# Kernel optimization log

Measured on AMD Instinct MI355X. Metric: run time of the kernel, lower is better.

The kernel has to match this reference:

```python
import jax, jax.numpy as jnp
import numpy as np

B, T, D = 2, 4096, 768
H = 12
DK = D // H


def setup_inputs() -> dict:
    key = jax.random.key(0)
    k1, k2, k3 = jax.random.split(key, 3)
    x = jax.random.normal(k1, (B, T, D), dtype=jnp.float32)
    W_qkv = jax.random.normal(k2, (D, 3 * D), dtype=jnp.float32) * (1.0 / np.sqrt(D))
    b_qkv = jnp.zeros((3 * D,), dtype=jnp.float32)
    W_proj = jax.random.normal(k3, (D, D), dtype=jnp.float32) * (1.0 / np.sqrt(D))
    b_proj = jnp.zeros((D,), dtype=jnp.float32)
    return {"x": x, "W_qkv": W_qkv, "b_qkv": b_qkv, "W_proj": W_proj, "b_proj": b_proj}


def reference(x, W_qkv, b_qkv, W_proj, b_proj):
    b, t, c = x.shape
    qkv = x @ W_qkv + b_qkv                      # [B,T,3D]
    q, k, v = jnp.split(qkv, 3, axis=-1)
    q = q.reshape(b, t, H, DK)                   # [B,T,H,DK]
    k = k.reshape(b, t, H, DK)
    v = v.reshape(b, t, H, DK)
    scale = 1.0 / np.sqrt(DK)
    scores = jnp.einsum('bthd,bshd->bhts', q, k) * scale   # [B,H,T,T]
    causal = jnp.tril(jnp.ones((t, t), dtype=bool))
    scores = jnp.where(causal[None, None], scores, jnp.float32(-jnp.inf))
    probs = jax.nn.softmax(scores, axis=-1)      # dropout p=0.0 -> identity
    out = jnp.einsum('bhts,bshd->bthd', probs, v).reshape(b, t, c)
    return out @ W_proj + b_proj
```

## Files before the change

### kernel.cpp

```cpp
#include <hip/hip_runtime.h>
#include <hip/hip_bf16.h>
#include <cstdint>
#include <cstddef>


typedef __attribute__((ext_vector_type(8))) short bf16x8;
typedef __attribute__((ext_vector_type(4))) float f32x4;

#define MFMA16(a, b, c) __builtin_amdgcn_mfma_f32_16x16x32_bf16((a), (b), (c), 0, 0, 0)

static constexpr int Bc = 2, Tc = 4096, Dc = 768, Hc = 12, DKc = 64;
static constexpr int BHc = Bc * Hc;
static constexpr int Mc = Bc * Tc;
static constexpr int Nqkv = 3 * Dc;
static constexpr int NQBLK = Tc / 128;
static constexpr unsigned int NITEMS = BHc * NQBLK;

__device__ __forceinline__ unsigned short f2bf(float f) {
    union { float f; unsigned int i; } c; c.f = f;
    unsigned int x = c.i;
    return (unsigned short)((x + 0x7fffu + ((x >> 16) & 1u)) >> 16);
}
__device__ __forceinline__ unsigned int pkbf(float a, float b) {
    __hip_bfloat162 h = __float22bfloat162_rn(make_float2(a, b));
    union { __hip_bfloat162 h; unsigned int u; } c; c.h = h;
    return c.u;
}

__global__ __launch_bounds__(256)
void xconv_kernel(const float* __restrict__ X, unsigned short* __restrict__ Xb) {
    size_t i = ((size_t)blockIdx.x * 256 + threadIdx.x) * 8;
    float4 a = *(const float4*)(X + i);
    float4 b = *(const float4*)(X + i + 4);
    uint4 o;
    o.x = pkbf(a.x, a.y); o.y = pkbf(a.z, a.w);
    o.z = pkbf(b.x, b.y); o.w = pkbf(b.z, b.w);
    *(uint4*)(Xb + i) = o;
}

__global__ __launch_bounds__(256)
void wtrans_kernel(const float* __restrict__ W, unsigned short* __restrict__ WT,
                   int K, int N) {
    __shared__ __align__(16) unsigned short tile[64 * 72];
    const int k0 = blockIdx.x * 64;
    const int n0 = blockIdx.y * 64;
    const int tid = threadIdx.x;
#pragma unroll
    for (int it = 0; it < 4; ++it) {
        int s = tid + it * 256;
        int r = s >> 4, g = s & 15;
        float4 v = *(const float4*)(W + (size_t)(k0 + r) * N + n0 + g * 4);
        ushort4 u;
        u.x = f2bf(v.x); u.y = f2bf(v.y); u.z = f2bf(v.z); u.w = f2bf(v.w);
        *(ushort4*)(tile + r * 72 + g * 4) = u;
    }
    __syncthreads();
#pragma unroll
    for (int it = 0; it < 2; ++it) {
        int s = tid + it * 256;
        int n = s >> 3, g = s & 7;
        unsigned int p0 = (unsigned int)tile[(g * 8 + 0) * 72 + n] |
                          ((unsigned int)tile[(g * 8 + 1) * 72 + n] << 16);
        unsigned int p1 = (unsigned int)tile[(g * 8 + 2) * 72 + n] |
                          ((unsigned int)tile[(g * 8 + 3) * 72 + n] << 16);
        unsigned int p2 = (unsigned int)tile[(g * 8 + 4) * 72 + n] |
                          ((unsigned int)tile[(g * 8 + 5) * 72 + n] << 16);
        unsigned int p3 = (unsigned int)tile[(g * 8 + 6) * 72 + n] |
                          ((unsigned int)tile[(g * 8 + 7) * 72 + n] << 16);
        uint4 o; o.x = p0; o.y = p1; o.z = p2; o.w = p3;
        *(uint4*)(WT + (size_t)(n0 + n) * K + k0 + g * 8) = o;
    }
}

__global__ __launch_bounds__(256)
void qkv_gemm_kernel(const unsigned short* __restrict__ Xb,
                     const unsigned short* __restrict__ WT,
                     const float* __restrict__ bias,
                     unsigned short* __restrict__ Qb, unsigned short* __restrict__ Kb,
                     unsigned short* __restrict__ Vt) {
    __shared__ __align__(16) unsigned short As[128 * 40];
    __shared__ __align__(16) unsigned short Bs[128 * 40];
    const int tid = threadIdx.x;
    const int wave = tid >> 6, lane = tid & 63;
    const int quad = lane >> 4, l15 = lane & 15;
    const int wr = wave >> 1, wc = wave & 1;
    const int r0 = blockIdx.x * 128, c0 = blockIdx.y * 128;

    f32x4 acc[4][4];
#pragma unroll
    for (int i = 0; i < 4; ++i)
#pragma unroll
        for (int j = 0; j < 4; ++j) acc[i][j] = (f32x4){0.f, 0.f, 0.f, 0.f};

    for (int k0 = 0; k0 < Dc; k0 += 32) {
#pragma unroll
        for (int it = 0; it < 2; ++it) {
            int s = tid + it * 256;
            int r = s >> 2, g = s & 3;
            *(uint4*)(As + r * 40 + g * 8) =
                *(const uint4*)(Xb + (size_t)(r0 + r) * Dc + k0 + g * 8);
            *(uint4*)(Bs + r * 40 + g * 8) =
                *(const uint4*)(WT + (size_t)(c0 + r) * Dc + k0 + g * 8);
        }
        __syncthreads();
        bf16x8 af[4], bfr[4];
#pragma unroll
        for (int mt = 0; mt < 4; ++mt)
            af[mt] = *(const bf16x8*)(As + (wr * 64 + mt * 16 + l15) * 40 + quad * 8);
#pragma unroll
        for (int nt = 0; nt < 4; ++nt)
            bfr[nt] = *(const bf16x8*)(Bs + (wc * 64 + nt * 16 + l15) * 40 + quad * 8);
#pragma unroll
        for (int mt = 0; mt < 4; ++mt)
#pragma unroll
            for (int nt = 0; nt < 4; ++nt)
                acc[mt][nt] = MFMA16(af[mt], bfr[nt], acc[mt][nt]);
        __syncthreads();
    }

    const int part = c0 / Dc;
    const int cbase = c0 - part * Dc;
    const float scale = (part == 0) ? 0.125f : 1.0f;
    float bv[4];
#pragma unroll
    for (int nt = 0; nt < 4; ++nt) bv[nt] = bias[c0 + wc * 64 + nt * 16 + l15];

    if (part < 2) {
        unsigned short* dstbuf = (part == 0) ? Qb : Kb;
#pragma unroll
        for (int mt = 0; mt < 4; ++mt)
#pragma unroll
            for (int reg = 0; reg < 4; ++reg) {
                int gr = r0 + wr * 64 + mt * 16 + quad * 4 + reg;
                int b = gr >> 12, t = gr & 4095;
#pragma unroll
                for (int nt = 0; nt < 4; ++nt) {
                    int cc = cbase + wc * 64 + nt * 16 + l15;
                    int h = cc >> 6, dk = cc & 63;
                    float v = (acc[mt][nt][reg] + bv[nt]) * scale;
                    dstbuf[((size_t)(b * Hc + h) * Tc + t) * DKc + dk] = f2bf(v);
                }
            }
    } else {
#pragma unroll
        for (int mt = 0; mt < 4; ++mt)
#pragma unroll
            for (int reg = 0; reg < 4; ++reg) {
                int gr = r0 + wr * 64 + mt * 16 + quad * 4 + reg;
                int b = gr >> 12, t = gr & 4095;
#pragma unroll
                for (int nt = 0; nt < 4; ++nt) {
                    int cc = cbase + wc * 64 + nt * 16 + l15;
                    int h = cc >> 6, dk = cc & 63;
                    float v = acc[mt][nt][reg] + bv[nt];
                    Vt[((size_t)(b * Hc + h) * DKc + dk) * Tc + t] = f2bf(v);
                }
            }
    }
}

__global__ __launch_bounds__(256)
void attn_kernel(const unsigned short* __restrict__ Qb,
                 const unsigned short* __restrict__ Kb,
                 const unsigned short* __restrict__ Vt,
                 unsigned short* __restrict__ attn,
                 unsigned int* __restrict__ counter) {
    __shared__ __align__(16) unsigned short Ks[64 * 72];
    __shared__ __align__(16) unsigned short Vs[64 * 72];
    __shared__ __align__(16) unsigned short Ps[4 * 16 * 72];
    __shared__ float Linv[128];
    __shared__ unsigned int s_w;
    const int tid = threadIdx.x;
    const int wave = tid >> 6, lane = tid & 63;
    const int quad = lane >> 4, l15 = lane & 15;
    const int rr = tid >> 3, gg = tid & 7;
    unsigned short* Pw = Ps + wave * 16 * 72;

    for (;;) {
        if (tid == 0) s_w = atomicAdd(counter, 1u);
        __syncthreads();
        const unsigned int w = s_w;
        if (w >= NITEMS) break;
        const int bh = (int)(w % (unsigned)BHc);
        const int i0 = (NQBLK - 1 - (int)(w / (unsigned)BHc)) * 128;
        const unsigned short* Qp = Qb + (size_t)bh * Tc * DKc;
        const unsigned short* Kp = Kb + (size_t)bh * Tc * DKc;
        const unsigned short* Vp = Vt + (size_t)bh * DKc * Tc;

        bf16x8 qf[2][2];
#pragma unroll
        for (int qg = 0; qg < 2; ++qg)
#pragma unroll
            for (int f = 0; f < 2; ++f)
                qf[qg][f] = *(const bf16x8*)(Qp +
                    (size_t)(i0 + wave * 32 + qg * 16 + l15) * DKc + f * 32 + quad * 8);

        f32x4 lp[2] = {(f32x4){0.f,0.f,0.f,0.f}, (f32x4){0.f,0.f,0.f,0.f}};
        f32x4 o[2][4];
#pragma unroll
        for (int qg = 0; qg < 2; ++qg)
#pragma unroll
            for (int nt = 0; nt < 4; ++nt) o[qg][nt] = (f32x4){0.f, 0.f, 0.f, 0.f};

        const int jmax = (i0 >> 6) + 1;
        for (int jt = 0; jt <= jmax; ++jt) {
            const int j0 = jt * 64;
#pragma unroll
            for (int it = 0; it < 2; ++it) {
                int r = rr + it * 32;
                *(uint4*)(Ks + r * 72 + gg * 8) =
                    *(const uint4*)(Kp + (size_t)(j0 + r) * DKc + gg * 8);
                *(uint4*)(Vs + r * 72 + gg * 8) =
                    *(const uint4*)(Vp + (size_t)r * Tc + j0 + gg * 8);
            }
            __syncthreads();

            bf16x8 kf[2][4], vf[2][4];
#pragma unroll
            for (int f = 0; f < 2; ++f)
#pragma unroll
                for (int mt = 0; mt < 4; ++mt)
                    kf[f][mt] = *(const bf16x8*)(Ks + (mt * 16 + l15) * 72 + f * 32 + quad * 8);
#pragma unroll
            for (int f = 0; f < 2; ++f)
#pragma unroll
                for (int nt = 0; nt < 4; ++nt)
                    vf[f][nt] = *(const bf16x8*)(Vs + (nt * 16 + l15) * 72 + f * 32 + quad * 8);

            const int rel = j0 - i0;
            const bool maskit = (jt >= jmax - 1);
#pragma unroll
            for (int qg = 0; qg < 2; ++qg) {
                f32x4 sc[4];
#pragma unroll
                for (int mt = 0; mt < 4; ++mt) sc[mt] = (f32x4){0.f, 0.f, 0.f, 0.f};
#pragma unroll
                for (int f = 0; f < 2; ++f)
#pragma unroll
                    for (int mt = 0; mt < 4; ++mt)
                        sc[mt] = MFMA16(kf[f][mt], qf[qg][f], sc[mt]);

                if (maskit) {
                    int qrow = wave * 32 + qg * 16 + l15;
#pragma unroll
                    for (int mt = 0; mt < 4; ++mt)
#pragma unroll
                        for (int reg = 0; reg < 4; ++reg)
                            if (rel + mt * 16 + quad * 4 + reg > qrow)
                                sc[mt][reg] = -1e30f;
                }

#pragma unroll
                for (int mt = 0; mt < 4; ++mt) {
#pragma unroll
                    for (int reg = 0; reg < 4; ++reg)
                        sc[mt][reg] = __expf(sc[mt][reg]);
                    lp[qg] += sc[mt];
                }

#pragma unroll
                for (int mt = 0; mt < 4; ++mt) {
                    uint2 u;
                    u.x = pkbf(sc[mt][0], sc[mt][1]);
                    u.y = pkbf(sc[mt][2], sc[mt][3]);
                    *(uint2*)(Pw + l15 * 72 + mt * 16 + quad * 4) = u;
                }

#pragma unroll
                for (int f = 0; f < 2; ++f) {
                    bf16x8 pf = *(const bf16x8*)(Pw + l15 * 72 + f * 32 + quad * 8);
#pragma unroll
                    for (int nt = 0; nt < 4; ++nt)
                        o[qg][nt] = MFMA16(pf, vf[f][nt], o[qg][nt]);
                }
            }
            __syncthreads();
        }

#pragma unroll
        for (int qg = 0; qg < 2; ++qg) {
            float ls = lp[qg][0] + lp[qg][1] + lp[qg][2] + lp[qg][3];
            ls += __shfl_xor(ls, 16);
            ls += __shfl_xor(ls, 32);
            Linv[wave * 32 + qg * 16 + l15] = 1.0f / ls;
        }

        const int b = bh / Hc, h = bh % Hc;
#pragma unroll
        for (int qg = 0; qg < 2; ++qg) {
            f32x4 li = *(const f32x4*)(Linv + wave * 32 + qg * 16 + quad * 4);
#pragma unroll
            for (int nt = 0; nt < 4; ++nt)
#pragma unroll
                for (int reg = 0; reg < 4; ++reg) {
                    int t = i0 + wave * 32 + qg * 16 + quad * 4 + reg;
                    attn[(size_t)(b * Tc + t) * Dc + h * 64 + nt * 16 + l15] =
                        f2bf(o[qg][nt][reg] * li[reg]);
                }
        }
        __syncthreads();
    }
}

__global__ __launch_bounds__(256)
void proj_gemm_kernel(const unsigned short* __restrict__ A,
                      const unsigned short* __restrict__ WT,
                      const float* __restrict__ bias, float* __restrict__ out) {
    __shared__ __align__(16) unsigned short As[128 * 40];
    __shared__ __align__(16) unsigned short Bs[128 * 40];
    const int tid = threadIdx.x;
    const int wave = tid >> 6, lane = tid & 63;
    const int quad = lane >> 4, l15 = lane & 15;
    const int wr = wave >> 1, wc = wave & 1;
    const int r0 = blockIdx.x * 128, c0 = blockIdx.y * 128;

    f32x4 acc[4][4];
#pragma unroll
    for (int i = 0; i < 4; ++i)
#pragma unroll
        for (int j = 0; j < 4; ++j) acc[i][j] = (f32x4){0.f, 0.f, 0.f, 0.f};

    for (int k0 = 0; k0 < Dc; k0 += 32) {
#pragma unroll
        for (int it = 0; it < 2; ++it) {
            int s = tid + it * 256;
            int r = s >> 2, g = s & 3;
            *(uint4*)(As + r * 40 + g * 8) =
                *(const uint4*)(A + (size_t)(r0 + r) * Dc + k0 + g * 8);
            *(uint4*)(Bs + r * 40 + g * 8) =
                *(const uint4*)(WT + (size_t)(c0 + r) * Dc + k0 + g * 8);
        }
        __syncthreads();
        bf16x8 af[4], bfr[4];
#pragma unroll
        for (int mt = 0; mt < 4; ++mt)
            af[mt] = *(const bf16x8*)(As + (wr * 64 + mt * 16 + l15) * 40 + quad * 8);
#pragma unroll
        for (int nt = 0; nt < 4; ++nt)
            bfr[nt] = *(const bf16x8*)(Bs + (wc * 64 + nt * 16 + l15) * 40 + quad * 8);
#pragma unroll
        for (int mt = 0; mt < 4; ++mt)
#pragma unroll
            for (int nt = 0; nt < 4; ++nt)
                acc[mt][nt] = MFMA16(af[mt], bfr[nt], acc[mt][nt]);
        __syncthreads();
    }

    float bv[4];
#pragma unroll
    for (int nt = 0; nt < 4; ++nt) bv[nt] = bias[c0 + wc * 64 + nt * 16 + l15];
#pragma unroll
    for (int mt = 0; mt < 4; ++mt)
#pragma unroll
        for (int reg = 0; reg < 4; ++reg) {
            int gr = r0 + wr * 64 + mt * 16 + quad * 4 + reg;
#pragma unroll
            for (int nt = 0; nt < 4; ++nt) {
                int gc = c0 + wc * 64 + nt * 16 + l15;
                out[(size_t)gr * Dc + gc] = acc[mt][nt][reg] + bv[nt];
            }
        }
}

extern "C" void kernel_launch(void* const* d_in, const int* in_sizes, int n_in,
                              void* d_out, int out_size, void* d_ws, size_t ws_size,
                              hipStream_t stream) {
    const float* x      = (const float*)d_in[0];
    const float* W_qkv  = (const float*)d_in[1];
    const float* b_qkv  = (const float*)d_in[2];
    const float* W_proj = (const float*)d_in[3];
    const float* b_proj = (const float*)d_in[4];
    float* out = (float*)d_out;

    char* ws = (char*)d_ws;
    size_t off = 0;
    auto take = [&](size_t bytes) -> char* {
        char* p = ws + off;
        off += (bytes + 255) & ~(size_t)255;
        return p;
    };
    unsigned int*   cnt = (unsigned int*)take(256);
    unsigned short* WqT = (unsigned short*)take((size_t)Nqkv * Dc * 2);
    unsigned short* WpT = (unsigned short*)take((size_t)Dc * Dc * 2);
    unsigned short* Qb  = (unsigned short*)take((size_t)BHc * Tc * DKc * 2);
    unsigned short* Kb  = (unsigned short*)take((size_t)BHc * Tc * DKc * 2);
    unsigned short* Vt  = (unsigned short*)take((size_t)BHc * Tc * DKc * 2);
    unsigned short* Xb  = (unsigned short*)take((size_t)Mc * Dc * 2);
    unsigned short* An  = Xb;

    hipMemsetAsync(cnt, 0, sizeof(unsigned int), stream);
    xconv_kernel<<<dim3((Mc * Dc) / (256 * 8)), dim3(256), 0, stream>>>(x, Xb);
    wtrans_kernel<<<dim3(Dc / 64, Nqkv / 64), dim3(256), 0, stream>>>(W_qkv, WqT, Dc, Nqkv);
    wtrans_kernel<<<dim3(Dc / 64, Dc / 64), dim3(256), 0, stream>>>(W_proj, WpT, Dc, Dc);
    qkv_gemm_kernel<<<dim3(Mc / 128, Nqkv / 128), dim3(256), 0, stream>>>(Xb, WqT, b_qkv, Qb, Kb, Vt);
    attn_kernel<<<dim3(NITEMS), dim3(256), 0, stream>>>(Qb, Kb, Vt, An, cnt);
    proj_gemm_kernel<<<dim3(Mc / 128, Dc / 128), dim3(256), 0, stream>>>(An, WpT, b_proj, out);
}
```

Before: 291.3 us.

## Make attention wave-independent with register-resident P and direct global K/V loads

Restructures the attention kernel so each wave pulls its own 32-query work item from the atomic counter and loads K and V fragments straight from global memory. This removes shared-memory staging and all block barriers. The P matrix now stays in registers and feeds a 16x16x16 MFMA with V as the A operand, avoiding the LDS round trip. Log2(e) is folded into the Q scale so exp2 replaces expf, and launch bounds request 3 blocks per CU. The trade-off is that K/V reuse across waves now relies on cache instead of LDS, which raises global/L2 traffic.

Measured after the change: 603.6 us. 107% more time.

```diff
diff --git a/kernel.cpp b/kernel.cpp
--- a/kernel.cpp
+++ b/kernel.cpp
@@ -5,16 +5,17 @@
 
 
 typedef __attribute__((ext_vector_type(8))) short bf16x8;
+typedef __attribute__((ext_vector_type(4))) short bf16x4;
 typedef __attribute__((ext_vector_type(4))) float f32x4;
 
-#define MFMA16(a, b, c) __builtin_amdgcn_mfma_f32_16x16x32_bf16((a), (b), (c), 0, 0, 0)
+#define MFMA16(a, b, c)   __builtin_amdgcn_mfma_f32_16x16x32_bf16((a), (b), (c), 0, 0, 0)
+#define MFMA16K(a, b, c)  __builtin_amdgcn_mfma_f32_16x16x16bf16_1k((a), (b), (c), 0, 0, 0)
 
 static constexpr int Bc = 2, Tc = 4096, Dc = 768, Hc = 12, DKc = 64;
 static constexpr int BHc = Bc * Hc;
 static constexpr int Mc = Bc * Tc;
 static constexpr int Nqkv = 3 * Dc;
-static constexpr int NQBLK = Tc / 128;
-static constexpr unsigned int NITEMS = BHc * NQBLK;
+static constexpr unsigned int NITEMS = BHc * (Tc / 32);
 
 __device__ __forceinline__ unsigned short f2bf(float f) {
     union { float f; unsigned int i; } c; c.f = f;
@@ -120,7 +121,7 @@
 
     const int part = c0 / Dc;
     const int cbase = c0 - part * Dc;
-    const float scale = (part == 0) ? 0.125f : 1.0f;
+    const float scale = (part == 0) ? 0.125f * 1.4426950408889634f : 1.0f;
     float bv[4];
 #pragma unroll
     for (int nt = 0; nt < 4; ++nt) bv[nt] = bias[c0 + wc * 64 + nt * 16 + l15];
@@ -159,30 +160,22 @@
     }
 }
 
-__global__ __launch_bounds__(256)
+__global__ __launch_bounds__(256, 3)
 void attn_kernel(const unsigned short* __restrict__ Qb,
                  const unsigned short* __restrict__ Kb,
                  const unsigned short* __restrict__ Vt,
                  unsigned short* __restrict__ attn,
                  unsigned int* __restrict__ counter) {
-    __shared__ __align__(16) unsigned short Ks[64 * 72];
-    __shared__ __align__(16) unsigned short Vs[64 * 72];
-    __shared__ __align__(16) unsigned short Ps[4 * 16 * 72];
-    __shared__ float Linv[128];
-    __shared__ unsigned int s_w;
-    const int tid = threadIdx.x;
-    const int wave = tid >> 6, lane = tid & 63;
+    const int lane = threadIdx.x & 63;
     const int quad = lane >> 4, l15 = lane & 15;
-    const int rr = tid >> 3, gg = tid & 7;
-    unsigned short* Pw = Ps + wave * 16 * 72;
 
     for (;;) {
-        if (tid == 0) s_w = atomicAdd(counter, 1u);
-        __syncthreads();
-        const unsigned int w = s_w;
+        unsigned int w = 0;
+        if (lane == 0) w = atomicAdd(counter, 1u);
+        w = (unsigned int)__shfl((int)w, 0);
         if (w >= NITEMS) break;
         const int bh = (int)(w % (unsigned)BHc);
-        const int i0 = (NQBLK - 1 - (int)(w / (unsigned)BHc)) * 128;
+        const int i0 = (Tc / 32 - 1 - (int)(w / (unsigned)BHc)) * 32;
         const unsigned short* Qp = Qb + (size_t)bh * Tc * DKc;
         const unsigned short* Kp = Kb + (size_t)bh * Tc * DKc;
         const unsigned short* Vp = Vt + (size_t)bh * DKc * Tc;
@@ -193,112 +186,89 @@
 #pragma unroll
             for (int f = 0; f < 2; ++f)
                 qf[qg][f] = *(const bf16x8*)(Qp +
-                    (size_t)(i0 + wave * 32 + qg * 16 + l15) * DKc + f * 32 + quad * 8);
+                    (size_t)(i0 + qg * 16 + l15) * DKc + f * 32 + quad * 8);
 
         f32x4 lp[2] = {(f32x4){0.f,0.f,0.f,0.f}, (f32x4){0.f,0.f,0.f,0.f}};
         f32x4 o[2][4];
 #pragma unroll
         for (int qg = 0; qg < 2; ++qg)
 #pragma unroll
-            for (int nt = 0; nt < 4; ++nt) o[qg][nt] = (f32x4){0.f, 0.f, 0.f, 0.f};
-
-        const int jmax = (i0 >> 6) + 1;
+            for (int d = 0; d < 4; ++d) o[qg][d] = (f32x4){0.f, 0.f, 0.f, 0.f};
+
+        const int jmax = i0 >> 6;
         for (int jt = 0; jt <= jmax; ++jt) {
             const int j0 = jt * 64;
-#pragma unroll
-            for (int it = 0; it < 2; ++it) {
-                int r = rr + it * 32;
-                *(uint4*)(Ks + r * 72 + gg * 8) =
-                    *(const uint4*)(Kp + (size_t)(j0 + r) * DKc + gg * 8);
-                *(uint4*)(Vs + r * 72 + gg * 8) =
-                    *(const uint4*)(Vp + (size_t)r * Tc + j0 + gg * 8);
-            }
-            __syncthreads();
-
-            bf16x8 kf[2][4], vf[2][4];
+
+            f32x4 sc[2][4];
+#pragma unroll
+            for (int qg = 0; qg < 2; ++qg)
+#pragma unroll
+                for (int mt = 0; mt < 4; ++mt) sc[qg][mt] = (f32x4){0.f, 0.f, 0.f, 0.f};
 #pragma unroll
             for (int f = 0; f < 2; ++f)
 #pragma unroll
-                for (int mt = 0; mt < 4; ++mt)
-                    kf[f][mt] = *(const bf16x8*)(Ks + (mt * 16 + l15) * 72 + f * 32 + quad * 8);
-#pragma unroll
-            for (int f = 0; f < 2; ++f)
-#pragma unroll
-                for (int nt = 0; nt < 4; ++nt)
-                    vf[f][nt] = *(const bf16x8*)(Vs + (nt * 16 + l15) * 72 + f * 32 + quad * 8);
-
-            const int rel = j0 - i0;
-            const bool maskit = (jt >= jmax - 1);
-#pragma unroll
-            for (int qg = 0; qg < 2; ++qg) {
-                f32x4 sc[4];
-#pragma unroll
-                for (int mt = 0; mt < 4; ++mt) sc[mt] = (f32x4){0.f, 0.f, 0.f, 0.f};
-#pragma unroll
-                for (int f = 0; f < 2; ++f)
+                for (int mt = 0; mt < 4; ++mt) {
+                    bf16x8 kf = *(const bf16x8*)(Kp +
+                        (size_t)(j0 + mt * 16 + l15) * DKc + f * 32 + quad * 8);
+                    sc[0][mt] = MFMA16(kf, qf[0][f], sc[0][mt]);
+                    sc[1][mt] = MFMA16(kf, qf[1][f], sc[1][mt]);
+                }
+
+            if (jt == jmax) {
+#pragma unroll
+                for (int qg = 0; qg < 2; ++qg)
 #pragma unroll
                     for (int mt = 0; mt < 4; ++mt)
-                        sc[mt] = MFMA16(kf[f][mt], qf[qg][f], sc[mt]);
-
-                if (maskit) {
-                    int qrow = wave * 32 + qg * 16 + l15;
-#pragma unroll
-                    for (int mt = 0; mt < 4; ++mt)
 #pragma unroll
                         for (int reg = 0; reg < 4; ++reg)
-                            if (rel + mt * 16 + quad * 4 + reg > qrow)
-                                sc[mt][reg] = -1e30f;
-                }
-
+                            if (j0 + mt * 16 + quad * 4 + reg > i0 + qg * 16 + l15)
+                                sc[qg][mt][reg] = -1e30f;
+            }
+
+            uint2 pb[2][4];
+#pragma unroll
+            for (int qg = 0; qg < 2; ++qg)
 #pragma unroll
                 for (int mt = 0; mt < 4; ++mt) {
 #pragma unroll
                     for (int reg = 0; reg < 4; ++reg)
-                        sc[mt][reg] = __expf(sc[mt][reg]);
-                    lp[qg] += sc[mt];
-                }
-
-#pragma unroll
-                for (int mt = 0; mt < 4; ++mt) {
-                    uint2 u;
-                    u.x = pkbf(sc[mt][0], sc[mt][1]);
-                    u.y = pkbf(sc[mt][2], sc[mt][3]);
-                    *(uint2*)(Pw + l15 * 72 + mt * 16 + quad * 4) = u;
-                }
-
-#pragma unroll
-                for (int f = 0; f < 2; ++f) {
-                    bf16x8 pf = *(const bf16x8*)(Pw + l15 * 72 + f * 32 + quad * 8);
-#pragma unroll
-                    for (int nt = 0; nt < 4; ++nt)
-                        o[qg][nt] = MFMA16(pf, vf[f][nt], o[qg][nt]);
-                }
-            }
-            __syncthreads();
-        }
-
+                        sc[qg][mt][reg] = __builtin_amdgcn_exp2f(sc[qg][mt][reg]);
+                    lp[qg] += sc[qg][mt];
+                    pb[qg][mt].x = pkbf(sc[qg][mt][0], sc[qg][mt][1]);
+                    pb[qg][mt].y = pkbf(sc[qg][mt][2], sc[qg][mt][3]);
+                }
+
+#pragma unroll
+            for (int mt = 0; mt < 4; ++mt) {
+                union { uint2 u; bf16x4 v; } b0, b1;
+                b0.u = pb[0][mt]; b1.u = pb[1][mt];
+#pragma unroll
+                for (int d = 0; d < 4; ++d) {
+                    bf16x4 vf = *(const bf16x4*)(Vp +
+                        (size_t)(d * 16 + l15) * Tc + j0 + mt * 16 + quad * 4);
+                    o[0][d] = MFMA16K(vf, b0.v, o[0][d]);
+                    o[1][d] = MFMA16K(vf, b1.v, o[1][d]);
+                }
+            }
+        }
+
+        const int b = bh / Hc, h = bh % Hc;
 #pragma unroll
         for (int qg = 0; qg < 2; ++qg) {
             float ls = lp[qg][0] + lp[qg][1] + lp[qg][2] + lp[qg][3];
             ls += __shfl_xor(ls, 16);
             ls += __shfl_xor(ls, 32);
-            Linv[wave * 32 + qg * 16 + l15] = 1.0f / ls;
-        }
-
-        const int b = bh / Hc, h = bh % Hc;
-#pragma unroll
-        for (int qg = 0; qg < 2; ++qg) {
-            f32x4 li = *(const f32x4*)(Linv + wave * 32 + qg * 16 + quad * 4);
-#pragma unroll
-            for (int nt = 0; nt < 4; ++nt)
-#pragma unroll
-                for (int reg = 0; reg < 4; ++reg) {
-                    int t = i0 + wave * 32 + qg * 16 + quad * 4 + reg;
-                    attn[(size_t)(b * Tc + t) * Dc + h * 64 + nt * 16 + l15] =
-                        f2bf(o[qg][nt][reg] * li[reg]);
-                }
-        }
-        __syncthreads();
+            float li = 1.0f / ls;
+            int t = i0 + qg * 16 + l15;
+            unsigned short* dst = attn + (size_t)(b * Tc + t) * Dc + h * 64;
+#pragma unroll
+            for (int d = 0; d < 4; ++d) {
+                uint2 u;
+                u.x = pkbf(o[qg][d][0] * li, o[qg][d][1] * li);
+                u.y = pkbf(o[qg][d][2] * li, o[qg][d][3] * li);
+                *(uint2*)(dst + d * 16 + quad * 4) = u;
+            }
+        }
     }
 }
 
@@ -393,6 +363,6 @@
     wtrans_kernel<<<dim3(Dc / 64, Nqkv / 64), dim3(256), 0, stream>>>(W_qkv, WqT, Dc, Nqkv);
     wtrans_kernel<<<dim3(Dc / 64, Dc / 64), dim3(256), 0, stream>>>(W_proj, WpT, Dc, Dc);
     qkv_gemm_kernel<<<dim3(Mc / 128, Nqkv / 128), dim3(256), 0, stream>>>(Xb, WqT, b_qkv, Qb, Kb, Vt);
-    attn_kernel<<<dim3(NITEMS), dim3(256), 0, stream>>>(Qb, Kb, Vt, An, cnt);
+    attn_kernel<<<dim3(NITEMS / 4), dim3(256), 0, stream>>>(Qb, Kb, Vt, An, cnt);
     proj_gemm_kernel<<<dim3(Mc / 128, Dc / 128), dim3(256), 0, stream>>>(An, WpT, b_proj, out);
 }
```

## Keep attention probabilities in registers via transposed PV MFMA and exp2

Applied to the files above, without the earlier changes.

Computes O^T = V^T P^T with 16x16x16 bf16 MFMAs so the exp'd score fragments from the QK^T MFMA feed the PV MFMA directly from registers, removing the per-wave LDS round trip for P. Folds log2(e) into the Q scale and uses exp2, interleaves the two query groups' MFMAs, moves the tile barrier to right after the fragment loads, and writes the output row-wise without the Linv LDS buffer. This trades LDS traffic and barriers for more V fragment registers and smaller-K MFMAs. Like the code before, there is no running max in the softmax.

Measured after the change: 274.5 us. 5.8% less time.

```diff
diff --git a/kernel.cpp b/kernel.cpp
--- a/kernel.cpp
+++ b/kernel.cpp
@@ -5,9 +5,11 @@
 
 
 typedef __attribute__((ext_vector_type(8))) short bf16x8;
+typedef __attribute__((ext_vector_type(4))) short bf16x4;
 typedef __attribute__((ext_vector_type(4))) float f32x4;
 
-#define MFMA16(a, b, c) __builtin_amdgcn_mfma_f32_16x16x32_bf16((a), (b), (c), 0, 0, 0)
+#define MFMA16(a, b, c)   __builtin_amdgcn_mfma_f32_16x16x32_bf16((a), (b), (c), 0, 0, 0)
+#define MFMA16K(a, b, c)  __builtin_amdgcn_mfma_f32_16x16x16bf16_1k((a), (b), (c), 0, 0, 0)
 
 static constexpr int Bc = 2, Tc = 4096, Dc = 768, Hc = 12, DKc = 64;
 static constexpr int BHc = Bc * Hc;
@@ -120,7 +122,7 @@
 
     const int part = c0 / Dc;
     const int cbase = c0 - part * Dc;
-    const float scale = (part == 0) ? 0.125f : 1.0f;
+    const float scale = (part == 0) ? 0.125f * 1.4426950408889634f : 1.0f;
     float bv[4];
 #pragma unroll
     for (int nt = 0; nt < 4; ++nt) bv[nt] = bias[c0 + wc * 64 + nt * 16 + l15];
@@ -167,14 +169,11 @@
                  unsigned int* __restrict__ counter) {
     __shared__ __align__(16) unsigned short Ks[64 * 72];
     __shared__ __align__(16) unsigned short Vs[64 * 72];
-    __shared__ __align__(16) unsigned short Ps[4 * 16 * 72];
-    __shared__ float Linv[128];
     __shared__ unsigned int s_w;
     const int tid = threadIdx.x;
     const int wave = tid >> 6, lane = tid & 63;
     const int quad = lane >> 4, l15 = lane & 15;
     const int rr = tid >> 3, gg = tid & 7;
-    unsigned short* Pw = Ps + wave * 16 * 72;
 
     for (;;) {
         if (tid == 0) s_w = atomicAdd(counter, 1u);
@@ -200,7 +199,7 @@
 #pragma unroll
         for (int qg = 0; qg < 2; ++qg)
 #pragma unroll
-            for (int nt = 0; nt < 4; ++nt) o[qg][nt] = (f32x4){0.f, 0.f, 0.f, 0.f};
+            for (int d = 0; d < 4; ++d) o[qg][d] = (f32x4){0.f, 0.f, 0.f, 0.f};
 
         const int jmax = (i0 >> 6) + 1;
         for (int jt = 0; jt <= jmax; ++jt) {
@@ -215,90 +214,86 @@
             }
             __syncthreads();
 
-            bf16x8 kf[2][4], vf[2][4];
+            bf16x8 kf[2][4];
+            bf16x4 vf[4][4];
 #pragma unroll
             for (int f = 0; f < 2; ++f)
 #pragma unroll
                 for (int mt = 0; mt < 4; ++mt)
                     kf[f][mt] = *(const bf16x8*)(Ks + (mt * 16 + l15) * 72 + f * 32 + quad * 8);
 #pragma unroll
+            for (int d = 0; d < 4; ++d)
+#pragma unroll
+                for (int mt = 0; mt < 4; ++mt)
+                    vf[d][mt] = *(const bf16x4*)(Vs + (d * 16 + l15) * 72 + mt * 16 + quad * 4);
+            __syncthreads();
+
+            f32x4 sc[2][4];
+#pragma unroll
+            for (int qg = 0; qg < 2; ++qg)
+#pragma unroll
+                for (int mt = 0; mt < 4; ++mt) sc[qg][mt] = (f32x4){0.f, 0.f, 0.f, 0.f};
+#pragma unroll
             for (int f = 0; f < 2; ++f)
 #pragma unroll
-                for (int nt = 0; nt < 4; ++nt)
-                    vf[f][nt] = *(const bf16x8*)(Vs + (nt * 16 + l15) * 72 + f * 32 + quad * 8);
+                for (int mt = 0; mt < 4; ++mt) {
+                    sc[0][mt] = MFMA16(kf[f][mt], qf[0][f], sc[0][mt]);
+                    sc[1][mt] = MFMA16(kf[f][mt], qf[1][f], sc[1][mt]);
+                }
 
             const int rel = j0 - i0;
-            const bool maskit = (jt >= jmax - 1);
-#pragma unroll
-            for (int qg = 0; qg < 2; ++qg) {
-                f32x4 sc[4];
-#pragma unroll
-                for (int mt = 0; mt < 4; ++mt) sc[mt] = (f32x4){0.f, 0.f, 0.f, 0.f};
-#pragma unroll
-                for (int f = 0; f < 2; ++f)
-#pragma unroll
-                    for (int mt = 0; mt < 4; ++mt)
-                        sc[mt] = MFMA16(kf[f][mt], qf[qg][f], sc[mt]);
-
-                if (maskit) {
+            if (jt >= jmax - 1) {
+#pragma unroll
+                for (int qg = 0; qg < 2; ++qg) {
                     int qrow = wave * 32 + qg * 16 + l15;
 #pragma unroll
                     for (int mt = 0; mt < 4; ++mt)
 #pragma unroll
                         for (int reg = 0; reg < 4; ++reg)
                             if (rel + mt * 16 + quad * 4 + reg > qrow)
-                                sc[mt][reg] = -1e30f;
-                }
-
+                                sc[qg][mt][reg] = -1e30f;
+                }
+            }
+
+            union { uint2 u; bf16x4 v; } pb[2][4];
+#pragma unroll
+            for (int qg = 0; qg < 2; ++qg)
 #pragma unroll
                 for (int mt = 0; mt < 4; ++mt) {
 #pragma unroll
                     for (int reg = 0; reg < 4; ++reg)
-                        sc[mt][reg] = __expf(sc[mt][reg]);
-                    lp[qg] += sc[mt];
-                }
-
-#pragma unroll
-                for (int mt = 0; mt < 4; ++mt) {
-                    uint2 u;
-                    u.x = pkbf(sc[mt][0], sc[mt][1]);
-                    u.y = pkbf(sc[mt][2], sc[mt][3]);
-                    *(uint2*)(Pw + l15 * 72 + mt * 16 + quad * 4) = u;
-                }
-
-#pragma unroll
-                for (int f = 0; f < 2; ++f) {
-                    bf16x8 pf = *(const bf16x8*)(Pw + l15 * 72 + f * 32 + quad * 8);
-#pragma unroll
-                    for (int nt = 0; nt < 4; ++nt)
-                        o[qg][nt] = MFMA16(pf, vf[f][nt], o[qg][nt]);
-                }
-            }
-            __syncthreads();
-        }
-
+                        sc[qg][mt][reg] = __builtin_amdgcn_exp2f(sc[qg][mt][reg]);
+                    lp[qg] += sc[qg][mt];
+                    pb[qg][mt].u.x = pkbf(sc[qg][mt][0], sc[qg][mt][1]);
+                    pb[qg][mt].u.y = pkbf(sc[qg][mt][2], sc[qg][mt][3]);
+                }
+
+#pragma unroll
+            for (int mt = 0; mt < 4; ++mt)
+#pragma unroll
+                for (int d = 0; d < 4; ++d) {
+                    o[0][d] = MFMA16K(vf[d][mt], pb[0][mt].v, o[0][d]);
+                    o[1][d] = MFMA16K(vf[d][mt], pb[1][mt].v, o[1][d]);
+                }
+        }
+
+        const int b = bh / Hc, h = bh % Hc;
 #pragma unroll
         for (int qg = 0; qg < 2; ++qg) {
             float ls = lp[qg][0] + lp[qg][1] + lp[qg][2] + lp[qg][3];
             ls += __shfl_xor(ls, 16);
             ls += __shfl_xor(ls, 32);
-            Linv[wave * 32 + qg * 16 + l15] = 1.0f / ls;
-        }
-
-        const int b = bh / Hc, h = bh % Hc;
-#pragma unroll
-        for (int qg = 0; qg < 2; ++qg) {
-            f32x4 li = *(const f32x4*)(Linv + wave * 32 + qg * 16 + quad * 4);
-#pragma unroll
-            for (int nt = 0; nt < 4; ++nt)
-#pragma unroll
-                for (int reg = 0; reg < 4; ++reg) {
-                    int t = i0 + wave * 32 + qg * 16 + quad * 4 + reg;
-                    attn[(size_t)(b * Tc + t) * Dc + h * 64 + nt * 16 + l15] =
-                        f2bf(o[qg][nt][reg] * li[reg]);
-                }
-        }
-        __syncthreads();
+            float li = 1.0f / ls;
+            int t = i0 + wave * 32 + qg * 16 + l15;
+            unsigned short* dst = attn + (size_t)(b * Tc + t) * Dc + h * 64;
+#pragma unroll
+            for (int d = 0; d < 4; ++d) {
+                uint2 u;
+                u.x = pkbf(o[qg][d][0] * li, o[qg][d][1] * li);
+                u.y = pkbf(o[qg][d][2] * li, o[qg][d][3] * li);
+                *(uint2*)(dst + d * 16 + quad * 4) = u;
+            }
+        }
     }
 }
 
```
